# Optimization experiments

Hardware: AMD Instinct MI355X
Metric: run time of the kernel (lower is better)

Reference implementation:

```python
import jax, jax.numpy as jnp
import numpy as np

B, T, N, M = 8, 4, 1024, 4096
C_IN, C_ORIG = 256, 128
P1, P2 = 256, 256
EPS_D = 1e-8   # three_nn inverse-distance epsilon
EPS_BN = 1e-5  # torch BatchNorm1d default eps


def setup_inputs() -> dict:
    key = jax.random.key(0)
    ks = jax.random.split(key, 6)
    return {
        "xyzs": jax.random.normal(ks[0], (B, T, N, 3), dtype=jnp.float32),
        "original_xyzs": jax.random.normal(ks[1], (B, T, M, 3), dtype=jnp.float32),
        "features": jax.random.normal(ks[2], (B, T, C_IN, N), dtype=jnp.float32),
        "original_features": jax.random.normal(ks[3], (B, T, C_ORIG, M), dtype=jnp.float32),
        "W1": jax.random.normal(ks[4], (P1, C_IN + C_ORIG), dtype=jnp.float32) * 0.05,
        "gamma1": jnp.ones((P1,), jnp.float32),
        "beta1": jnp.zeros((P1,), jnp.float32),
        "W2": jax.random.normal(ks[5], (P2, P1), dtype=jnp.float32) * 0.05,
        "gamma2": jnp.ones((P2,), jnp.float32),
        "beta2": jnp.zeros((P2,), jnp.float32),
    }


def _three_nn_interpolate(xyzs, orig_xyzs, feats):
    # squared pairwise distances, as the pointnet2 three_nn kernel returns d^2
    # d2: [B,T,M,N]
    d2 = jnp.sum((orig_xyzs[:, :, :, None, :] - xyzs[:, :, None, :, :]) ** 2, axis=-1)
    neg, idx = jax.lax.top_k(-d2, 3)           # 3 nearest; idx: [B,T,M,3]
    dist = -neg
    w = 1.0 / (dist + EPS_D)
    w = w / jnp.sum(w, axis=-1, keepdims=True)  # [B,T,M,3]
    b, t, c, n = feats.shape
    m = idx.shape[2]
    # gather neighbor features: [B,T,C,M,3]
    g = jnp.take_along_axis(feats, idx.reshape(b, t, 1, m * 3), axis=3)
    g = g.reshape(b, t, c, m, 3)
    return jnp.einsum("btcmk,btmk->btcm", g, w)


def _bn_per_frame(x, gamma, beta):
    # torch training-mode BN applied per frame t: stats over (B, M) per (t, c)
    mean = jnp.mean(x, axis=(0, 3), keepdims=True)
    var = jnp.var(x, axis=(0, 3), keepdims=True)  # biased, matches torch normalization
    xh = (x - mean) * jax.lax.rsqrt(var + EPS_BN)
    return gamma[None, None, :, None] * xh + beta[None, None, :, None]


def reference(xyzs, original_xyzs, features, original_features,
              W1, gamma1, beta1, W2, gamma2, beta2):
    interp = _three_nn_interpolate(xyzs, original_xyzs, features)     # [B,T,C_IN,M]
    x = jnp.concatenate([interp, original_features], axis=2)          # [B,T,C_IN+C_ORIG,M]
    x = jnp.einsum("oc,btcm->btom", W1, x)                            # 1x1 conv, no bias
    x = jax.nn.relu(_bn_per_frame(x, gamma1, beta1))
    x = jnp.einsum("oc,btcm->btom", W2, x)
    x = jax.nn.relu(_bn_per_frame(x, gamma2, beta2))
    return original_xyzs, x
```

## Files before the change

kernel.cpp:

```cpp
#include <hip/hip_runtime.h>
#include <hip/hip_bf16.h>

#define Bb 8
#define Tt 4
#define Nn 1024
#define Mm 4096
#define BT 32
#define CIN 256
#define CORIG 128
#define CTOT 384
#define P1 256
#define P2 256
#define EPS_D 1e-8f
#define EPS_BN 1e-5f

typedef __attribute__((ext_vector_type(4))) float f32x4;
typedef __attribute__((ext_vector_type(8))) short s16x8;

__device__ __forceinline__ unsigned short f2bf(float f) {
    unsigned int u = __float_as_uint(f);
    unsigned int r = (u + 0x7FFFu + ((u >> 16) & 1u)) >> 16;
    return (unsigned short)r;
}
__device__ __forceinline__ float bf2f(unsigned short b) {
    return __uint_as_float((unsigned int)b << 16);
}
__device__ __forceinline__ void split_bf16(float f, unsigned short& h, unsigned short& l) {
    h = f2bf(f);
    l = f2bf(f - bf2f(h));
}

__global__ __launch_bounds__(256) void prep_w_kernel(
    const float* __restrict__ W, unsigned short* __restrict__ hi,
    unsigned short* __restrict__ lo, int total)
{
    int i = blockIdx.x * 256 + threadIdx.x;
    if (i < total) {
        unsigned short h, l;
        split_bf16(W[i], h, l);
        hi[i] = h; lo[i] = l;
    }
}

__global__ __launch_bounds__(256) void three_nn_kernel(
    const float* __restrict__ xyzs,
    const float* __restrict__ oxyzs,
    int*   __restrict__ idx_out,
    float* __restrict__ w_out)
{
    __shared__ float sx[Nn], sy[Nn], sz[Nn];
    int bt = blockIdx.y;
    const float* base = xyzs + (size_t)bt * Nn * 3;
    for (int i = threadIdx.x; i < Nn; i += 256) {
        sx[i] = base[i * 3 + 0];
        sy[i] = base[i * 3 + 1];
        sz[i] = base[i * 3 + 2];
    }
    __syncthreads();

    int m = blockIdx.x * 256 + threadIdx.x;
    size_t q = ((size_t)bt * Mm + m) * 3;
    float qx = oxyzs[q + 0], qy = oxyzs[q + 1], qz = oxyzs[q + 2];

    float d0 = 3.4e38f, d1 = 3.4e38f, d2v = 3.4e38f;
    int   i0 = 0, i1 = 0, i2 = 0;
    #pragma unroll 4
    for (int n = 0; n < Nn; n++) {
        float dx = qx - sx[n], dy = qy - sy[n], dz = qz - sz[n];
        float d = dx * dx + dy * dy + dz * dz;
        bool lt0 = d < d0, lt1 = d < d1, lt2 = d < d2v;
        i2  = lt1 ? i1 : (lt2 ? n : i2);
        d2v = lt1 ? d1 : (lt2 ? d : d2v);
        i1  = lt0 ? i0 : (lt1 ? n : i1);
        d1  = lt0 ? d0 : (lt1 ? d : d1);
        i0  = lt0 ? n : i0;
        d0  = lt0 ? d : d0;
    }
    float w0 = 1.0f / (d0 + EPS_D);
    float w1 = 1.0f / (d1 + EPS_D);
    float w2 = 1.0f / (d2v + EPS_D);
    float inv = 1.0f / (w0 + w1 + w2);
    idx_out[q + 0] = i0; idx_out[q + 1] = i1; idx_out[q + 2] = i2;
    w_out[q + 0] = w0 * inv; w_out[q + 1] = w1 * inv; w_out[q + 2] = w2 * inv;
}

__global__ __launch_bounds__(256) void transpose_feats_kernel(
    const float* __restrict__ feats, float* __restrict__ featsT)
{
    __shared__ float tile[64][65];
    int bt = blockIdx.z;
    int n0 = blockIdx.x * 64;
    int c0 = blockIdx.y * 64;
    int tx = threadIdx.x & 63;
    int ty = threadIdx.x >> 6;
    const float* src = feats + ((size_t)bt * CIN + c0) * Nn + n0;
    #pragma unroll
    for (int r = 0; r < 16; r++) {
        int c = ty + r * 4;
        tile[c][tx] = src[(size_t)c * Nn + tx];
    }
    __syncthreads();
    float* dst = featsT + ((size_t)bt * Nn + n0) * CIN + c0;
    #pragma unroll
    for (int r = 0; r < 16; r++) {
        int n = ty + r * 4;
        dst[(size_t)n * CIN + tx] = tile[tx][n];
    }
}

__global__ __launch_bounds__(256) void interp_kernel(
    const float* __restrict__ featsT,
    const int*   __restrict__ idx,
    const float* __restrict__ w,
    float* __restrict__ Xi)
{
    __shared__ float sX[256][33];
    __shared__ int   sidx[96];
    __shared__ float swgt[96];
    int bt = blockIdx.y;
    int m0 = blockIdx.x * 32;
    int tid = threadIdx.x;
    size_t base = ((size_t)bt * Mm + m0) * 3;
    if (tid < 96)       sidx[tid]      = idx[base + tid];
    else if (tid < 192) swgt[tid - 96] = w[base + tid - 96];
    __syncthreads();

    const float* fb = featsT + (size_t)bt * Nn * CIN + tid;
    #pragma unroll 4
    for (int mm = 0; mm < 32; mm++) {
        int   j0 = sidx[mm * 3 + 0], j1 = sidx[mm * 3 + 1], j2 = sidx[mm * 3 + 2];
        float w0 = swgt[mm * 3 + 0], w1 = swgt[mm * 3 + 1], w2 = swgt[mm * 3 + 2];
        sX[tid][mm] = w0 * fb[(size_t)j0 * CIN]
                    + w1 * fb[(size_t)j1 * CIN]
                    + w2 * fb[(size_t)j2 * CIN];
    }
    __syncthreads();

    float* xb = Xi + (size_t)bt * CIN * Mm + m0;
    #pragma unroll
    for (int i = 0; i < 8; i++) {
        int row = i * 32 + (tid >> 3);
        int col = (tid & 7) * 4;
        float4 v = make_float4(sX[row][col], sX[row][col + 1],
                               sX[row][col + 2], sX[row][col + 3]);
        *(float4*)&xb[(size_t)row * Mm + col] = v;
    }
}

template <int KTOT, bool TRANSFORM, bool CONCAT>
__global__ __launch_bounds__(256) void mfma_gemm_kernel(
    const unsigned short* __restrict__ Whi,
    const unsigned short* __restrict__ Wlo,
    const float* __restrict__ Xg,
    const float* __restrict__ OF,
    const float* __restrict__ stats,
    float* __restrict__ Y)
{
    __shared__ unsigned short sAhi[128][40];
    __shared__ unsigned short sAlo[128][40];
    __shared__ unsigned short sBhi[128][40];
    __shared__ unsigned short sBlo[128][40];

    const int tid = threadIdx.x;
    const int bt = blockIdx.z, t = bt & (Tt - 1);
    const int m0 = blockIdx.x * 128, o0 = blockIdx.y * 128;

    const int mo = tid & 127;
    const int kh = tid >> 7;
    const float* Xb  = Xg + (size_t)bt * (CONCAT ? CIN : KTOT) * Mm + m0 + mo;
    const float* OFb = CONCAT ? (OF + (size_t)bt * CORIG * Mm + m0 + mo) : nullptr;

    const int lane = tid & 63, wid = tid >> 6;
    const int wo = (wid >> 1) * 64, wm = (wid & 1) * 64;
    const int lr = lane & 15, kb = lane >> 4;

    f32x4 acc[4][4] = {};

    for (int k0 = 0; k0 < KTOT; k0 += 32) {
        {
            const uint4* ph = (const uint4*)&Whi[(size_t)(o0 + mo) * KTOT + k0 + kh * 16];
            const uint4* pl = (const uint4*)&Wlo[(size_t)(o0 + mo) * KTOT + k0 + kh * 16];
            uint4 h0 = ph[0], h1 = ph[1];
            uint4 l0 = pl[0], l1 = pl[1];
            *(uint4*)&sAhi[mo][kh * 16]     = h0;
            *(uint4*)&sAhi[mo][kh * 16 + 8] = h1;
            *(uint4*)&sAlo[mo][kh * 16]     = l0;
            *(uint4*)&sAlo[mo][kh * 16 + 8] = l1;
        }
        {
            const int kg = k0 + kh * 16;
            const float* bsrc = (CONCAT && kg >= CIN)
                              ? (OFb + (size_t)(kg - CIN) * Mm)
                              : (Xb + (size_t)kg * Mm);
            float v[16];
            #pragma unroll
            for (int kk = 0; kk < 16; kk++)
                v[kk] = bsrc[(size_t)kk * Mm];
            if (TRANSFORM) {
                #pragma unroll
                for (int kk = 0; kk < 16; kk++) {
                    int k = kg + kk;
                    float a = stats[(t * KTOT + k) * 2 + 0];
                    float b = stats[(t * KTOT + k) * 2 + 1];
                    v[kk] = fmaxf(fmaf(a, v[kk], b), 0.0f);
                }
            }
            s16x8 H0, H1, L0, L1;
            #pragma unroll
            for (int kk = 0; kk < 8; kk++) {
                unsigned short h, l;
                split_bf16(v[kk], h, l);
                H0[kk] = (short)h; L0[kk] = (short)l;
                split_bf16(v[kk + 8], h, l);
                H1[kk] = (short)h; L1[kk] = (short)l;
            }
            *(s16x8*)&sBhi[mo][kh * 16]     = H0;
            *(s16x8*)&sBhi[mo][kh * 16 + 8] = H1;
            *(s16x8*)&sBlo[mo][kh * 16]     = L0;
            *(s16x8*)&sBlo[mo][kh * 16 + 8] = L1;
        }
        __syncthreads();

        s16x8 ah[4], al[4], bh[4], bl[4];
        #pragma unroll
        for (int f = 0; f < 4; f++) {
            ah[f] = *(const s16x8*)&sAhi[wo + f * 16 + lr][kb * 8];
            al[f] = *(const s16x8*)&sAlo[wo + f * 16 + lr][kb * 8];
            bh[f] = *(const s16x8*)&sBhi[wm + f * 16 + lr][kb * 8];
            bl[f] = *(const s16x8*)&sBlo[wm + f * 16 + lr][kb * 8];
        }
        #pragma unroll
        for (int fo = 0; fo < 4; fo++) {
            #pragma unroll
            for (int fn = 0; fn < 4; fn++) {
                acc[fo][fn] = __builtin_amdgcn_mfma_f32_16x16x32_bf16(ah[fo], bh[fn], acc[fo][fn], 0, 0, 0);
                acc[fo][fn] = __builtin_amdgcn_mfma_f32_16x16x32_bf16(ah[fo], bl[fn], acc[fo][fn], 0, 0, 0);
                acc[fo][fn] = __builtin_amdgcn_mfma_f32_16x16x32_bf16(al[fo], bh[fn], acc[fo][fn], 0, 0, 0);
            }
        }
        __syncthreads();
    }

    float* Yb = Y + (size_t)bt * 256 * Mm;
    #pragma unroll
    for (int fo = 0; fo < 4; fo++) {
        int obase = o0 + wo + fo * 16 + kb * 4;
        #pragma unroll
        for (int r = 0; r < 4; r++) {
            float* row = &Yb[(size_t)(obase + r) * Mm + m0 + wm + lr];
            #pragma unroll
            for (int fn = 0; fn < 4; fn++)
                row[fn * 16] = acc[fo][fn][r];
        }
    }
}

__global__ __launch_bounds__(256) void bn_stats_kernel(
    const float* __restrict__ Y,
    const float* __restrict__ gamma,
    const float* __restrict__ beta,
    float* __restrict__ stats)
{
    int o = blockIdx.x & 255;
    int t = blockIdx.x >> 8;
    int tid = threadIdx.x;
    float s1 = 0.0f, s2 = 0.0f;
    for (int b = 0; b < Bb; b++) {
        const float* row = Y + ((size_t)(b * Tt + t) * 256 + o) * Mm;
        for (int m = tid * 4; m < Mm; m += 1024) {
            float4 v = *(const float4*)&row[m];
            s1 += v.x + v.y + v.z + v.w;
            s2 += v.x * v.x + v.y * v.y + v.z * v.z + v.w * v.w;
        }
    }
    #pragma unroll
    for (int off = 32; off > 0; off >>= 1) {
        s1 += __shfl_down(s1, off);
        s2 += __shfl_down(s2, off);
    }
    __shared__ float r1[4], r2[4];
    int wv = tid >> 6;
    if ((tid & 63) == 0) { r1[wv] = s1; r2[wv] = s2; }
    __syncthreads();
    if (tid == 0) {
        float S1 = r1[0] + r1[1] + r1[2] + r1[3];
        float S2 = r2[0] + r2[1] + r2[2] + r2[3];
        const float inv = 1.0f / (float)(Bb * Mm);
        float mean = S1 * inv;
        float var  = S2 * inv - mean * mean;
        float a = gamma[o] * rsqrtf(var + EPS_BN);
        stats[(t * 256 + o) * 2 + 0] = a;
        stats[(t * 256 + o) * 2 + 1] = beta[o] - mean * a;
    }
}

__global__ __launch_bounds__(256) void bn_apply_kernel(
    const float* __restrict__ Y,
    const float* __restrict__ stats,
    float* __restrict__ out)
{
    size_t i4 = (size_t)blockIdx.x * 256 + threadIdx.x;
    size_t r = i4 >> 10;
    int o  = (int)(r & 255);
    int bt = (int)(r >> 8);
    int t  = bt & (Tt - 1);
    float a = stats[(t * 256 + o) * 2 + 0];
    float b = stats[(t * 256 + o) * 2 + 1];
    float4 v = *(const float4*)&Y[i4 * 4];
    v.x = fmaxf(fmaf(a, v.x, b), 0.0f);
    v.y = fmaxf(fmaf(a, v.y, b), 0.0f);
    v.z = fmaxf(fmaf(a, v.z, b), 0.0f);
    v.w = fmaxf(fmaf(a, v.w, b), 0.0f);
    *(float4*)&out[i4 * 4] = v;
}

extern "C" void kernel_launch(void* const* d_in, const int* in_sizes, int n_in,
                              void* d_out, int out_size, void* d_ws, size_t ws_size,
                              hipStream_t stream)
{
    const float* xyzs   = (const float*)d_in[0];
    const float* oxyzs  = (const float*)d_in[1];
    const float* feats  = (const float*)d_in[2];
    const float* ofeats = (const float*)d_in[3];
    const float* W1     = (const float*)d_in[4];
    const float* gamma1 = (const float*)d_in[5];
    const float* beta1  = (const float*)d_in[6];
    const float* W2     = (const float*)d_in[7];
    const float* gamma2 = (const float*)d_in[8];
    const float* beta2  = (const float*)d_in[9];
    float* out = (float*)d_out;

    char* ws = (char*)d_ws;
    int*            idx_ws = (int*)ws;
    float*          w_ws   = (float*)(ws + 1572864);
    unsigned short* Whi1   = (unsigned short*)(ws + 3145728);
    unsigned short* Wlo1   = (unsigned short*)(ws + 3342336);
    unsigned short* Whi2   = (unsigned short*)(ws + 3538944);
    unsigned short* Wlo2   = (unsigned short*)(ws + 3670016);
    float*          stats1 = (float*)(ws + 3801088);
    float*          stats2 = (float*)(ws + 3809280);
    float*          featsT = (float*)(ws + 4194304);
    float*          Xi     = (float*)(ws + 37748736);
    float*          Y1     = (float*)(ws + 171966464);
    float*          Y2     = Xi;

    hipMemcpyAsync(out, oxyzs, 393216 * sizeof(float),
                   hipMemcpyDeviceToDevice, stream);

    prep_w_kernel<<<(P1 * CTOT + 255) / 256, 256, 0, stream>>>(W1, Whi1, Wlo1, P1 * CTOT);
    prep_w_kernel<<<(P2 * P1 + 255) / 256, 256, 0, stream>>>(W2, Whi2, Wlo2, P2 * P1);

    three_nn_kernel<<<dim3(Mm / 256, BT), 256, 0, stream>>>(xyzs, oxyzs, idx_ws, w_ws);

    transpose_feats_kernel<<<dim3(Nn / 64, CIN / 64, BT), 256, 0, stream>>>(feats, featsT);
    interp_kernel<<<dim3(Mm / 32, BT), 256, 0, stream>>>(featsT, idx_ws, w_ws, Xi);

    mfma_gemm_kernel<CTOT, false, true><<<dim3(Mm / 128, 2, BT), 256, 0, stream>>>(
        Whi1, Wlo1, Xi, ofeats, nullptr, Y1);

    bn_stats_kernel<<<Tt * 256, 256, 0, stream>>>(Y1, gamma1, beta1, stats1);

    mfma_gemm_kernel<P1, true, false><<<dim3(Mm / 128, 2, BT), 256, 0, stream>>>(
        Whi2, Wlo2, Y1, nullptr, stats1, Y2);

    bn_stats_kernel<<<Tt * 256, 256, 0, stream>>>(Y2, gamma2, beta2, stats2);

    bn_apply_kernel<<<(BT * 256 * Mm / 4) / 256, 256, 0, stream>>>(
        Y2, stats2, out + 393216);
}
```

Measured before the change: 634.4 us.

## Fuse BN statistics into GEMM epilogue, prefetch tiles, pre-split interp output

```diff
diff --git a/kernel.cpp b/kernel.cpp
--- a/kernel.cpp
+++ b/kernel.cpp
@@ -29,6 +29,11 @@
     h = f2bf(f);
     l = f2bf(f - bf2f(h));
 }
+__device__ __forceinline__ unsigned int pack_bf(float f) {
+    unsigned short h, l;
+    split_bf16(f, h, l);
+    return ((unsigned int)h << 16) | (unsigned int)l;
+}
 
 __global__ __launch_bounds__(256) void prep_w_kernel(
     const float* __restrict__ W, unsigned short* __restrict__ hi,
@@ -40,6 +45,11 @@
         split_bf16(W[i], h, l);
         hi[i] = h; lo[i] = l;
     }
+}
+
+__global__ __launch_bounds__(256) void zero_stats_kernel(float* __restrict__ p)
+{
+    p[blockIdx.x * 256 + threadIdx.x] = 0.0f;
 }
 
 __global__ __launch_bounds__(256) void three_nn_kernel(
@@ -112,7 +122,7 @@
     const float* __restrict__ featsT,
     const int*   __restrict__ idx,
     const float* __restrict__ w,
-    float* __restrict__ Xi)
+    unsigned int* __restrict__ Xp)
 {
     __shared__ float sX[256][33];
     __shared__ int   sidx[96];
@@ -136,14 +146,17 @@
     }
     __syncthreads();
 
-    float* xb = Xi + (size_t)bt * CIN * Mm + m0;
+    unsigned int* xb = Xp + (size_t)bt * CIN * Mm + m0;
     #pragma unroll
     for (int i = 0; i < 8; i++) {
         int row = i * 32 + (tid >> 3);
         int col = (tid & 7) * 4;
-        float4 v = make_float4(sX[row][col], sX[row][col + 1],
-                               sX[row][col + 2], sX[row][col + 3]);
-        *(float4*)&xb[(size_t)row * Mm + col] = v;
+        uint4 v;
+        v.x = pack_bf(sX[row][col]);
+        v.y = pack_bf(sX[row][col + 1]);
+        v.z = pack_bf(sX[row][col + 2]);
+        v.w = pack_bf(sX[row][col + 3]);
+        *(uint4*)&xb[(size_t)row * Mm + col] = v;
     }
 }
 
@@ -151,15 +164,17 @@
 __global__ __launch_bounds__(256) void mfma_gemm_kernel(
     const unsigned short* __restrict__ Whi,
     const unsigned short* __restrict__ Wlo,
-    const float* __restrict__ Xg,
+    const unsigned int* __restrict__ Xg,
     const float* __restrict__ OF,
     const float* __restrict__ stats,
-    float* __restrict__ Y)
+    float* __restrict__ Y,
+    float* __restrict__ statsAcc)
 {
     __shared__ unsigned short sAhi[128][40];
     __shared__ unsigned short sAlo[128][40];
     __shared__ unsigned short sBhi[128][40];
     __shared__ unsigned short sBlo[128][40];
+    __shared__ float sStats[TRANSFORM ? 2 * KTOT : 2];
 
     const int tid = threadIdx.x;
     const int bt = blockIdx.z, t = bt & (Tt - 1);
@@ -167,59 +182,83 @@
 
     const int mo = tid & 127;
     const int kh = tid >> 7;
-    const float* Xb  = Xg + (size_t)bt * (CONCAT ? CIN : KTOT) * Mm + m0 + mo;
+    const unsigned int* Xb = Xg + (size_t)bt * (CONCAT ? CIN : KTOT) * Mm + m0 + mo;
     const float* OFb = CONCAT ? (OF + (size_t)bt * CORIG * Mm + m0 + mo) : nullptr;
 
     const int lane = tid & 63, wid = tid >> 6;
     const int wo = (wid >> 1) * 64, wm = (wid & 1) * 64;
     const int lr = lane & 15, kb = lane >> 4;
 
+    if (TRANSFORM) {
+        for (int i = tid; i < 2 * KTOT; i += 256)
+            sStats[i] = stats[t * KTOT * 2 + i];
+    }
+
     f32x4 acc[4][4] = {};
+    unsigned int rb[16];
+    uint4 ra0, ra1, ra2, ra3;
+
+    auto LOADA = [&](int k0_) {
+        const uint4* ph = (const uint4*)&Whi[(size_t)(o0 + mo) * KTOT + k0_ + kh * 16];
+        const uint4* pl = (const uint4*)&Wlo[(size_t)(o0 + mo) * KTOT + k0_ + kh * 16];
+        ra0 = ph[0]; ra1 = ph[1]; ra2 = pl[0]; ra3 = pl[1];
+    };
+    auto LOADB = [&](int k0_) {
+        const int kg = k0_ + kh * 16;
+        if (CONCAT && kg >= CIN) {
+            const float* p = OFb + (size_t)(kg - CIN) * Mm;
+            #pragma unroll
+            for (int kk = 0; kk < 16; kk++)
+                rb[kk] = __float_as_uint(p[(size_t)kk * Mm]);
+        } else {
+            const unsigned int* p = Xb + (size_t)kg * Mm;
+            #pragma unroll
+            for (int kk = 0; kk < 16; kk++)
+                rb[kk] = p[(size_t)kk * Mm];
+        }
+    };
+    auto STORE = [&](int k0_) {
+        const int kg = k0_ + kh * 16;
+        *(uint4*)&sAhi[mo][kh * 16]     = ra0;
+        *(uint4*)&sAhi[mo][kh * 16 + 8] = ra1;
+        *(uint4*)&sAlo[mo][kh * 16]     = ra2;
+        *(uint4*)&sAlo[mo][kh * 16 + 8] = ra3;
+        s16x8 H0, H1, L0, L1;
+        const bool packed = CONCAT && (kg < CIN);
+        #pragma unroll
+        for (int kk = 0; kk < 8; kk++) {
+            unsigned short h, l, h2, l2;
+            if (packed) {
+                unsigned int p = rb[kk], q = rb[kk + 8];
+                h  = (unsigned short)(p >> 16); l  = (unsigned short)(p & 0xFFFFu);
+                h2 = (unsigned short)(q >> 16); l2 = (unsigned short)(q & 0xFFFFu);
+            } else {
+                float v = __uint_as_float(rb[kk]);
+                float v2 = __uint_as_float(rb[kk + 8]);
+                if (TRANSFORM) {
+                    int k = kg + kk;
+                    v  = fmaxf(fmaf(sStats[k * 2],        v,  sStats[k * 2 + 1]),  0.0f);
+                    v2 = fmaxf(fmaf(sStats[(k + 8) * 2],  v2, sStats[(k + 8) * 2 + 1]), 0.0f);
+                }
+                split_bf16(v, h, l);
+                split_bf16(v2, h2, l2);
+            }
+            H0[kk] = (short)h;  L0[kk] = (short)l;
+            H1[kk] = (short)h2; L1[kk] = (short)l2;
+        }
+        *(s16x8*)&sBhi[mo][kh * 16]     = H0;
+        *(s16x8*)&sBhi[mo][kh * 16 + 8] = H1;
+        *(s16x8*)&sBlo[mo][kh * 16]     = L0;
+        *(s16x8*)&sBlo[mo][kh * 16 + 8] = L1;
+    };
+
+    LOADA(0); LOADB(0);
+    STORE(0);
+    __syncthreads();
 
     for (int k0 = 0; k0 < KTOT; k0 += 32) {
-        {
-            const uint4* ph = (const uint4*)&Whi[(size_t)(o0 + mo) * KTOT + k0 + kh * 16];
-            const uint4* pl = (const uint4*)&Wlo[(size_t)(o0 + mo) * KTOT + k0 + kh * 16];
-            uint4 h0 = ph[0], h1 = ph[1];
-            uint4 l0 = pl[0], l1 = pl[1];
-            *(uint4*)&sAhi[mo][kh * 16]     = h0;
-            *(uint4*)&sAhi[mo][kh * 16 + 8] = h1;
-            *(uint4*)&sAlo[mo][kh * 16]     = l0;
-            *(uint4*)&sAlo[mo][kh * 16 + 8] = l1;
-        }
-        {
-            const int kg = k0 + kh * 16;
-            const float* bsrc = (CONCAT && kg >= CIN)
-                              ? (OFb + (size_t)(kg - CIN) * Mm)
-                              : (Xb + (size_t)kg * Mm);
-            float v[16];
-            #pragma unroll
-            for (int kk = 0; kk < 16; kk++)
-                v[kk] = bsrc[(size_t)kk * Mm];
-            if (TRANSFORM) {
-                #pragma unroll
-                for (int kk = 0; kk < 16; kk++) {
-                    int k = kg + kk;
-                    float a = stats[(t * KTOT + k) * 2 + 0];
-                    float b = stats[(t * KTOT + k) * 2 + 1];
-                    v[kk] = fmaxf(fmaf(a, v[kk], b), 0.0f);
-                }
-            }
-            s16x8 H0, H1, L0, L1;
-            #pragma unroll
-            for (int kk = 0; kk < 8; kk++) {
-                unsigned short h, l;
-                split_bf16(v[kk], h, l);
-                H0[kk] = (short)h; L0[kk] = (short)l;
-                split_bf16(v[kk + 8], h, l);
-                H1[kk] = (short)h; L1[kk] = (short)l;
-            }
-            *(s16x8*)&sBhi[mo][kh * 16]     = H0;
-            *(s16x8*)&sBhi[mo][kh * 16 + 8] = H1;
-            *(s16x8*)&sBlo[mo][kh * 16]     = L0;
-            *(s16x8*)&sBlo[mo][kh * 16 + 8] = L1;
-        }
-        __syncthreads();
+        const bool more = (k0 + 32) < KTOT;
+        if (more) { LOADA(k0 + 32); LOADB(k0 + 32); }
 
         s16x8 ah[4], al[4], bh[4], bl[4];
         #pragma unroll
@@ -239,6 +278,10 @@
             }
         }
         __syncthreads();
+        if (more) {
+            STORE(k0 + 32);
+            __syncthreads();
+        }
     }
 
     float* Yb = Y + (size_t)bt * 256 * Mm;
@@ -253,45 +296,44 @@
                 row[fn * 16] = acc[fo][fn][r];
         }
     }
-}
-
-__global__ __launch_bounds__(256) void bn_stats_kernel(
-    const float* __restrict__ Y,
-    const float* __restrict__ gamma,
-    const float* __restrict__ beta,
-    float* __restrict__ stats)
-{
-    int o = blockIdx.x & 255;
-    int t = blockIdx.x >> 8;
-    int tid = threadIdx.x;
-    float s1 = 0.0f, s2 = 0.0f;
-    for (int b = 0; b < Bb; b++) {
-        const float* row = Y + ((size_t)(b * Tt + t) * 256 + o) * Mm;
-        for (int m = tid * 4; m < Mm; m += 1024) {
-            float4 v = *(const float4*)&row[m];
-            s1 += v.x + v.y + v.z + v.w;
-            s2 += v.x * v.x + v.y * v.y + v.z * v.z + v.w * v.w;
-        }
-    }
     #pragma unroll
-    for (int off = 32; off > 0; off >>= 1) {
-        s1 += __shfl_down(s1, off);
-        s2 += __shfl_down(s2, off);
-    }
-    __shared__ float r1[4], r2[4];
-    int wv = tid >> 6;
-    if ((tid & 63) == 0) { r1[wv] = s1; r2[wv] = s2; }
-    __syncthreads();
-    if (tid == 0) {
-        float S1 = r1[0] + r1[1] + r1[2] + r1[3];
-        float S2 = r2[0] + r2[1] + r2[2] + r2[3];
-        const float inv = 1.0f / (float)(Bb * Mm);
-        float mean = S1 * inv;
-        float var  = S2 * inv - mean * mean;
-        float a = gamma[o] * rsqrtf(var + EPS_BN);
-        stats[(t * 256 + o) * 2 + 0] = a;
-        stats[(t * 256 + o) * 2 + 1] = beta[o] - mean * a;
-    }
+    for (int fo = 0; fo < 4; fo++) {
+        #pragma unroll
+        for (int r = 0; r < 4; r++) {
+            float a1 = 0.0f, a2 = 0.0f;
+            #pragma unroll
+            for (int fn = 0; fn < 4; fn++) {
+                float v = acc[fo][fn][r];
+                a1 += v;
+                a2 += v * v;
+            }
+            #pragma unroll
+            for (int msk = 1; msk < 16; msk <<= 1) {
+                a1 += __shfl_xor(a1, msk);
+                a2 += __shfl_xor(a2, msk);
+            }
+            if (lr == 0) {
+                int o = o0 + wo + fo * 16 + kb * 4 + r;
+                atomicAdd(&statsAcc[(t * 256 + o) * 2 + 0], a1);
+                atomicAdd(&statsAcc[(t * 256 + o) * 2 + 1], a2);
+            }
+        }
+    }
+}
+
+__global__ __launch_bounds__(256) void finalize_stats_kernel(
+    float* __restrict__ acc, const float* __restrict__ gamma,
+    const float* __restrict__ beta)
+{
+    int i = blockIdx.x * 256 + threadIdx.x;
+    int o = i & 255;
+    float S1 = acc[i * 2], S2 = acc[i * 2 + 1];
+    const float inv = 1.0f / (float)(Bb * Mm);
+    float mean = S1 * inv;
+    float var  = S2 * inv - mean * mean;
+    float a = gamma[o] * rsqrtf(var + EPS_BN);
+    acc[i * 2]     = a;
+    acc[i * 2 + 1] = beta[o] - mean * a;
 }
 
 __global__ __launch_bounds__(256) void bn_apply_kernel(
@@ -337,34 +379,33 @@
     unsigned short* Wlo1   = (unsigned short*)(ws + 3342336);
     unsigned short* Whi2   = (unsigned short*)(ws + 3538944);
     unsigned short* Wlo2   = (unsigned short*)(ws + 3670016);
-    float*          stats1 = (float*)(ws + 3801088);
-    float*          stats2 = (float*)(ws + 3809280);
+    float*          sAcc1  = (float*)(ws + 3801088);
+    float*          sAcc2  = (float*)(ws + 3809280);
     float*          featsT = (float*)(ws + 4194304);
-    float*          Xi     = (float*)(ws + 37748736);
+    unsigned int*   Xp     = (unsigned int*)(ws + 37748736);
     float*          Y1     = (float*)(ws + 171966464);
-    float*          Y2     = Xi;
+    float*          Y2     = (float*)Xp;
 
     hipMemcpyAsync(out, oxyzs, 393216 * sizeof(float),
                    hipMemcpyDeviceToDevice, stream);
 
     prep_w_kernel<<<(P1 * CTOT + 255) / 256, 256, 0, stream>>>(W1, Whi1, Wlo1, P1 * CTOT);
     prep_w_kernel<<<(P2 * P1 + 255) / 256, 256, 0, stream>>>(W2, Whi2, Wlo2, P2 * P1);
+    zero_stats_kernel<<<16, 256, 0, stream>>>(sAcc1);
 
     three_nn_kernel<<<dim3(Mm / 256, BT), 256, 0, stream>>>(xyzs, oxyzs, idx_ws, w_ws);
 
     transpose_feats_kernel<<<dim3(Nn / 64, CIN / 64, BT), 256, 0, stream>>>(feats, featsT);
-    interp_kernel<<<dim3(Mm / 32, BT), 256, 0, stream>>>(featsT, idx_ws, w_ws, Xi);
+    interp_kernel<<<dim3(Mm / 32, BT), 256, 0, stream>>>(featsT, idx_ws, w_ws, Xp);
 
     mfma_gemm_kernel<CTOT, false, true><<<dim3(Mm / 128, 2, BT), 256, 0, stream>>>(
-        Whi1, Wlo1, Xi, ofeats, nullptr, Y1);
-
-    bn_stats_kernel<<<Tt * 256, 256, 0, stream>>>(Y1, gamma1, beta1, stats1);
+        Whi1, Wlo1, Xp, ofeats, nullptr, Y1, sAcc1);
+    finalize_stats_kernel<<<4, 256, 0, stream>>>(sAcc1, gamma1, beta1);
 
     mfma_gemm_kernel<P1, true, false><<<dim3(Mm / 128, 2, BT), 256, 0, stream>>>(
-        Whi2, Wlo2, Y1, nullptr, stats1, Y2);
-
-    bn_stats_kernel<<<Tt * 256, 256, 0, stream>>>(Y2, gamma2, beta2, stats2);
+        Whi2, Wlo2, (const unsigned int*)Y1, nullptr, sAcc1, Y2, sAcc2);
+    finalize_stats_kernel<<<4, 256, 0, stream>>>(sAcc2, gamma2, beta2);
 
     bn_apply_kernel<<<(BT * 256 * Mm / 4) / 256, 256, 0, stream>>>(
-        Y2, stats2, out + 393216);
-}
+        Y2, sAcc2, out + 393216);
+}
```

Result: slower. 758.4 us (+19.5%).
